# Performance work log

Measured on AMD Instinct MI355X. Metric: run time of the kernel, lower is better.

## Reference

```python
import jax, jax.numpy as jnp
import numpy as np

NUM_HEADS = 4
TEMPERATURE = 1.0
EDGE_WEIGHT = 0.5


def setup_inputs() -> dict:
    key = jax.random.key(0)
    k1, k2, k3 = jax.random.split(key, 3)
    x = jax.random.normal(k1, (4, 2048, 512), dtype=jnp.float32)
    gate_w = jax.random.normal(k2, (1, 1), dtype=jnp.float32)
    gate_b = jax.random.normal(k3, (1,), dtype=jnp.float32)
    return {"x": x, "gate_w": gate_w, "gate_b": gate_b}


def _forward(x, gate_w, gate_b):
    B, N, C = x.shape
    H = NUM_HEADS
    hd = C // H
    # F.normalize(x, dim=-1) with eps=1e-12
    norm = jnp.linalg.norm(x, axis=-1, keepdims=True)
    x_norm = x / jnp.maximum(norm, 1e-12)
    # multi-head cosine-sim attention
    xh = x_norm.reshape(B, N, H, hd).transpose(0, 2, 1, 3)  # (B,H,N,hd)
    sim = jnp.einsum("bhnd,bhmd->bhnm", xh, xh) / (hd ** 0.5 * TEMPERATURE)
    attn = jax.nn.softmax(sim, axis=-1)
    xv = x.reshape(B, N, H, hd).transpose(0, 2, 1, 3)  # (B,H,N,hd)
    x_refined = jnp.einsum("bhnm,bhmd->bhnd", attn, xv)
    x_refined = x_refined.transpose(0, 2, 1, 3).reshape(B, N, C)
    # edge-variance mask (no_grad in torch -> stop_gradient)
    diff = jnp.var(x, axis=-1, keepdims=True, ddof=1)  # (B,N,1), unbiased like torch
    edge_mask = jax.nn.sigmoid((diff - diff.mean()) / (jnp.std(diff, ddof=1) + 1e-6))
    edge_mask = jax.lax.stop_gradient(edge_mask)
    x_refined = (1.0 + EDGE_WEIGHT * edge_mask) * x_refined
    # scalar gate: Linear(1,1) + Sigmoid on global mean
    gate_input = x.mean(axis=1, keepdims=True).mean(axis=-1, keepdims=True)  # (B,1,1)
    gate = jax.nn.sigmoid(gate_input * gate_w[0, 0] + gate_b[0])
    x_refined = gate * x_refined
    return x + x_refined


def reference(x, gate_w, gate_b):
    return _forward(x, gate_w, gate_b)
```

## Files before the change

kernel.cpp:

```cpp
#include <hip/hip_runtime.h>
#include <stdint.h>

#define B_   4
#define N_   2048
#define C_   512
#define H_   4
#define HD_  128
#define BN_  (B_ * N_)
#define NIT_ 32
#define SCALE_LOG2E 0.1275129727595311f

typedef __attribute__((ext_vector_type(8))) short  short8;
typedef __attribute__((ext_vector_type(4))) unsigned short ushort4_t;
typedef __attribute__((ext_vector_type(4))) float  float4_t;
typedef __attribute__((ext_vector_type(8))) __bf16 bf16x8;

static __device__ __forceinline__ unsigned short f2bf(float f) {
  union { float f; uint32_t u; } v; v.f = f;
  uint32_t r = v.u + 0x7FFFu + ((v.u >> 16) & 1u);
  return (unsigned short)(r >> 16);
}

static __device__ __forceinline__ uint32_t cvtpk_bf16(float lo, float hi) {
  uint32_t r;
  asm("v_cvt_pk_bf16_f32 %0, %1, %2" : "=v"(r) : "v"(lo), "v"(hi));
  return r;
}

#if __has_builtin(__builtin_amdgcn_exp2f)
#define EXP2(x) __builtin_amdgcn_exp2f(x)
#else
#define EXP2(x) exp2f(x)
#endif

static __device__ __forceinline__ float4_t mfma16(short8 a, short8 b, float4_t c) {
  return __builtin_amdgcn_mfma_f32_16x16x32_bf16(
      __builtin_bit_cast(bf16x8, a), __builtin_bit_cast(bf16x8, b), c, 0, 0, 0);
}

#define GLOAD16(SRC, DST)                                               \
  __builtin_amdgcn_global_load_lds(                                     \
      (const __attribute__((address_space(1))) void*)(SRC),             \
      (__attribute__((address_space(3))) void*)(DST), 16, 0, 0)

__global__ __launch_bounds__(256) void k_stats(
    const float* __restrict__ x, unsigned short* __restrict__ xnq,
    float* __restrict__ diff, float* __restrict__ toksum) {
  int tok  = blockIdx.x * 4 + (threadIdx.x >> 6);
  int lane = threadIdx.x & 63;
  const float* xr = x + (size_t)tok * C_;
  float4_t a = *(const float4_t*)(xr + lane * 8);
  float4_t b = *(const float4_t*)(xr + lane * 8 + 4);
  float s = 0.f, ss = 0.f;
#pragma unroll
  for (int j = 0; j < 4; ++j) {
    s  += a[j] + b[j];
    ss += a[j] * a[j] + b[j] * b[j];
  }
#pragma unroll
  for (int o = 1; o < 64; o <<= 1) {
    s  += __shfl_xor(s, o);
    ss += __shfl_xor(ss, o);
  }
  float rn = 1.f / fmaxf(sqrtf(ss), 1e-12f);
  short8 o8;
#pragma unroll
  for (int j = 0; j < 4; ++j) {
    o8[j]     = (short)f2bf(a[j] * rn);
    o8[j + 4] = (short)f2bf(b[j] * rn);
  }
  *(short8*)(xnq + (size_t)tok * C_ + lane * 8) = o8;
  if (lane == 0) {
    diff[tok]   = (ss - s * s * (1.f / C_)) * (1.f / (C_ - 1));
    toksum[tok] = s;
  }
}

__global__ __launch_bounds__(256) void k_transpose(
    const float* __restrict__ x, unsigned short* __restrict__ xvT) {
  __shared__ float tr[HD_][65];
  int bh = blockIdx.x & 15, nt = blockIdx.x >> 4;
  int b = bh >> 2, h = bh & 3;
  int n0 = nt * 64, c0 = h * HD_;
  int t = threadIdx.x;
  int dm = (t & 31) * 4;
  int nr = t >> 5;
#pragma unroll
  for (int p = 0; p < 8; ++p) {
    int n = p * 8 + nr;
    float4_t v = *(const float4_t*)(x + ((size_t)(b * N_ + n0 + n)) * C_ + c0 + dm);
#pragma unroll
    for (int k = 0; k < 4; ++k) tr[dm + k][n] = v[k];
  }
  __syncthreads();
#pragma unroll
  for (int p = 0; p < 4; ++p) {
    int c = p * 256 + t;
    int d = c >> 3, nc = (c & 7) * 8;
    int P = ((d & 7) << 1) | ((d >> 3) & 1);
    int q0h = nc >> 2;
    ushort4_t h0, h1;
#pragma unroll
    for (int e = 0; e < 4; ++e) {
      h0[e] = f2bf(tr[d][nc + e]);
      h1[e] = f2bf(tr[d][nc + 4 + e]);
    }
    unsigned short* base = xvT + ((size_t)bh * HD_ + d) * N_ + n0;
    *(ushort4_t*)(base + (((q0h    ) ^ P) << 2)) = h0;
    *(ushort4_t*)(base + (((q0h + 1) ^ P) << 2)) = h1;
  }
}

__global__ __launch_bounds__(256) void k_finalize(
    const float* __restrict__ diff, const float* __restrict__ toksum,
    const float* __restrict__ gw, const float* __restrict__ gb,
    float* __restrict__ stats) {
  __shared__ float sh[4][8];
  int t = threadIdx.x, l = t & 63, w = t >> 6;
  float s1 = 0.f, s2 = 0.f;
  for (int i = t; i < BN_; i += 256) { float d = diff[i]; s1 += d; s2 += d * d; }
  float bs0 = 0.f, bs1 = 0.f, bs2 = 0.f, bs3 = 0.f;
  for (int i = t; i < N_; i += 256) {
    bs0 += toksum[i];          bs1 += toksum[N_ + i];
    bs2 += toksum[2 * N_ + i]; bs3 += toksum[3 * N_ + i];
  }
#pragma unroll
  for (int o = 1; o < 64; o <<= 1) {
    s1 += __shfl_xor(s1, o);  s2 += __shfl_xor(s2, o);
    bs0 += __shfl_xor(bs0, o); bs1 += __shfl_xor(bs1, o);
    bs2 += __shfl_xor(bs2, o); bs3 += __shfl_xor(bs3, o);
  }
  if (l == 0) {
    sh[w][0] = s1; sh[w][1] = s2;
    sh[w][2] = bs0; sh[w][3] = bs1; sh[w][4] = bs2; sh[w][5] = bs3;
  }
  __syncthreads();
  if (t == 0) {
    float S1 = sh[0][0] + sh[1][0] + sh[2][0] + sh[3][0];
    float S2 = sh[0][1] + sh[1][1] + sh[2][1] + sh[3][1];
    float mean = S1 / (float)BN_;
    float var  = (S2 - S1 * S1 / (float)BN_) / (float)(BN_ - 1);
    float rstd = 1.f / (sqrtf(var) + 1e-6f);
    stats[0] = mean; stats[1] = rstd;
    float w00 = gw[0], bb = gb[0];
#pragma unroll
    for (int q = 0; q < 4; ++q) {
      float bsum = sh[0][2 + q] + sh[1][2 + q] + sh[2][2 + q] + sh[3][2 + q];
      float gi = bsum / (float)(N_ * C_);
      stats[2 + q] = 1.f / (1.f + __expf(-(gi * w00 + bb)));
    }
  }
}

__global__ __launch_bounds__(256) void k_attn(
    const float* __restrict__ x, const unsigned short* __restrict__ xnq,
    const unsigned short* __restrict__ xvT, const float* __restrict__ diff,
    const float* __restrict__ stats, float* __restrict__ out) {
  __shared__ unsigned short sm[32768];
  int i  = blockIdx.x;
  int bh = ((i & 7) << 1) | ((i >> 3) & 1);
  int qt = i >> 4;
  int b = bh >> 2, h = bh & 3, c0 = h * HD_;
  int tid = threadIdx.x, w = tid >> 6, l = tid & 63;
  int g = l >> 4, r = l & 15;
  int r3 = (r >> 3) & 1;
  int q0 = qt * 64 + w * 16;

  short8 qf[4];
  const unsigned short* qbase = xnq + ((size_t)(b * N_ + q0)) * C_ + c0;
#pragma unroll
  for (int cs = 0; cs < 4; ++cs)
    qf[cs] = *(const short8*)(qbase + (size_t)r * C_ + g * 8 + cs * 32);

  float4_t acc[8];
  float ls = 0.f;
#pragma unroll
  for (int dt = 0; dt < 8; ++dt) acc[dt] = (float4_t){0.f, 0.f, 0.f, 0.f};

  auto stage = [&](int it, int cb) {
    const unsigned short* ks = xnq + ((size_t)(b * N_ + it * 64)) * C_ + c0;
    unsigned short* kd = &sm[cb * 8192];
#pragma unroll
    for (int jj = 0; jj < 4; ++jj) {
      int j = w * 4 + jj;
      int row = 4 * j + g;
      int ssl = r ^ (row & 15);
      GLOAD16(ks + (size_t)row * C_ + ssl * 8, kd + j * 512);
    }
    const unsigned short* vs = xvT + ((size_t)bh * HD_) * N_ + it * 64;
    unsigned short* vd = &sm[16384 + cb * 8192];
#pragma unroll
    for (int jj = 0; jj < 4; ++jj) {
      int j = w * 4 + jj;
      int d = 8 * j + (l >> 3);
      GLOAD16(vs + (size_t)d * N_ + (l & 7) * 8, vd + j * 512);
    }
  };

  stage(0, 0);
  __syncthreads();

  for (int it = 0; it < NIT_; ++it) {
    int cb = it & 1;
    if (it + 1 < NIT_) stage(it + 1, cb ^ 1);
    const unsigned short* K = &sm[cb * 8192];
    const unsigned short* V = &sm[16384 + cb * 8192];

    float4_t p[4];
#pragma unroll
    for (int t4 = 0; t4 < 4; ++t4) p[t4] = (float4_t){0.f, 0.f, 0.f, 0.f};

    __builtin_amdgcn_s_setprio(1);
#pragma unroll
    for (int t4 = 0; t4 < 4; ++t4) {
#pragma unroll
      for (int cs = 0; cs < 4; ++cs) {
        short8 kf = *(const short8*)(K + (size_t)(t4 * 16 + r) * 128 +
                                     ((g * 8 + cs * 32) ^ (r * 8)));
        p[t4] = mfma16(kf, qf[cs], p[t4]);
      }
    }
    __builtin_amdgcn_s_setprio(0);

    union { short8 s8; uint32_t u[4]; } pf[2];
#pragma unroll
    for (int t4 = 0; t4 < 4; ++t4) {
      float e0 = EXP2(p[t4][0] * SCALE_LOG2E);
      float e1 = EXP2(p[t4][1] * SCALE_LOG2E);
      float e2 = EXP2(p[t4][2] * SCALE_LOG2E);
      float e3 = EXP2(p[t4][3] * SCALE_LOG2E);
      ls += (e0 + e1) + (e2 + e3);
      pf[t4 >> 1].u[(t4 & 1) * 2 + 0] = cvtpk_bf16(e0, e1);
      pf[t4 >> 1].u[(t4 & 1) * 2 + 1] = cvtpk_bf16(e2, e3);
    }

    int X = ((r & 7) << 3) | (r3 << 2);
    __builtin_amdgcn_s_setprio(1);
#pragma unroll
    for (int dt = 0; dt < 8; ++dt) {
      const unsigned short* vrow = V + (size_t)(dt * 16 + r) * 64;
      union { short8 s8; ushort4_t h[2]; } vf0, vf1;
      vf0.h[0] = *(const ushort4_t*)(vrow + ((g * 4)      ^ X));
      vf0.h[1] = *(const ushort4_t*)(vrow + ((g * 4 + 16) ^ X));
      vf1.h[0] = *(const ushort4_t*)(vrow + ((g * 4 + 32) ^ X));
      vf1.h[1] = *(const ushort4_t*)(vrow + ((g * 4 + 48) ^ X));
      acc[dt] = mfma16(vf0.s8, pf[0].s8, acc[dt]);
      acc[dt] = mfma16(vf1.s8, pf[1].s8, acc[dt]);
    }
    __builtin_amdgcn_s_setprio(0);
    __syncthreads();
  }

  ls += __shfl_xor(ls, 16);
  ls += __shfl_xor(ls, 32);
  float mean = stats[0], rstd = stats[1], gate = stats[2 + b];
  int q = q0 + r;
  float dv = diff[b * N_ + q];
  float em = 1.f / (1.f + __expf(-(dv - mean) * rstd));
  float f  = gate * (1.f + 0.5f * em) / ls;
  const float* xr = x + ((size_t)(b * N_ + q)) * C_;
  float* orow = out + ((size_t)(b * N_ + q)) * C_;
#pragma unroll
  for (int dt = 0; dt < 8; ++dt) {
    int dcol = c0 + dt * 16 + g * 4;
    float4_t xin = *(const float4_t*)(xr + dcol);
    float4_t o;
#pragma unroll
    for (int j = 0; j < 4; ++j) o[j] = xin[j] + f * acc[dt][j];
    *(float4_t*)(orow + dcol) = o;
  }
}

extern "C" void kernel_launch(void* const* d_in, const int* in_sizes, int n_in,
                              void* d_out, int out_size, void* d_ws, size_t ws_size,
                              hipStream_t stream) {
  (void)in_sizes; (void)n_in; (void)out_size; (void)ws_size;
  const float* x  = (const float*)d_in[0];
  const float* gw = (const float*)d_in[1];
  const float* gb = (const float*)d_in[2];
  float* out = (float*)d_out;
  unsigned short* xnq = (unsigned short*)d_ws;
  unsigned short* xvT = xnq + (size_t)BN_ * C_;
  float* diff   = (float*)(xvT + (size_t)BN_ * C_);
  float* toksum = diff + BN_;
  float* stats  = toksum + BN_;
  hipLaunchKernelGGL(k_stats, dim3(BN_ / 4), dim3(256), 0, stream, x, xnq, diff, toksum);
  hipLaunchKernelGGL(k_transpose, dim3(512), dim3(256), 0, stream, x, xvT);
  hipLaunchKernelGGL(k_finalize, dim3(1), dim3(256), 0, stream, diff, toksum, gw, gb, stats);
  hipLaunchKernelGGL(k_attn, dim3(512), dim3(256), 0, stream, x, xnq, xvT, diff, stats, out);
}
```

Before: 77.43 us.

## Restructure attention to two waves with register-resident K and key-split reduction

The attention kernel now uses 128 threads per block. Each wave owns all 64 queries of the tile and handles a 32-key half, loading K fragments straight from global memory into registers rather than staging them through LDS. Only V is double-buffered in LDS, with a new swizzle that allows single 16-byte reads, and the transpose kernel writes V in that matching layout. The two waves' partial accumulators and row sums are combined through LDS at the end. The aim is more MFMA work per fragment load and less LDS traffic, at the cost of much higher register pressure, lower occupancy from launch_bounds(128,1), and an extra reduction step.

```diff
diff --git a/kernel.cpp b/kernel.cpp
--- a/kernel.cpp
+++ b/kernel.cpp
@@ -94,20 +94,16 @@
   }
   __syncthreads();
 #pragma unroll
-  for (int p = 0; p < 4; ++p) {
-    int c = p * 256 + t;
-    int d = c >> 3, nc = (c & 7) * 8;
-    int P = ((d & 7) << 1) | ((d >> 3) & 1);
-    int q0h = nc >> 2;
-    ushort4_t h0, h1;
-#pragma unroll
-    for (int e = 0; e < 4; ++e) {
-      h0[e] = f2bf(tr[d][nc + e]);
-      h1[e] = f2bf(tr[d][nc + 4 + e]);
-    }
-    unsigned short* base = xvT + ((size_t)bh * HD_ + d) * N_ + n0;
-    *(ushort4_t*)(base + (((q0h    ) ^ P) << 2)) = h0;
-    *(ushort4_t*)(base + (((q0h + 1) ^ P) << 2)) = h1;
+  for (int p4 = 0; p4 < 4; ++p4) {
+    int c = p4 * 256 + t;
+    int d = c >> 3, pb = c & 7;
+    int lg = pb ^ (d & 7);
+    int kbase = 32 * (lg >> 2) + 4 * (lg & 3);
+    short8 o8;
+#pragma unroll
+    for (int e = 0; e < 8; ++e)
+      o8[e] = (short)f2bf(tr[d][kbase + 16 * (e >> 2) + (e & 3)]);
+    *(short8*)(xvT + ((size_t)(bh * HD_ + d)) * N_ + n0 + pb * 8) = o8;
   }
 }
 
@@ -152,122 +148,193 @@
   }
 }
 
-__global__ __launch_bounds__(256) void k_attn(
+__global__ __launch_bounds__(128, 1) void k_attn(
     const float* __restrict__ x, const unsigned short* __restrict__ xnq,
     const unsigned short* __restrict__ xvT, const float* __restrict__ diff,
     const float* __restrict__ stats, float* __restrict__ out) {
-  __shared__ unsigned short sm[32768];
+  __shared__ unsigned short sm[16384];
   int i  = blockIdx.x;
   int bh = ((i & 7) << 1) | ((i >> 3) & 1);
   int qt = i >> 4;
   int b = bh >> 2, h = bh & 3, c0 = h * HD_;
   int tid = threadIdx.x, w = tid >> 6, l = tid & 63;
   int g = l >> 4, r = l & 15;
-  int r3 = (r >> 3) & 1;
-  int q0 = qt * 64 + w * 16;
-
-  short8 qf[4];
+  int q0 = qt * 64;
+
+  short8 qf[4][4];
   const unsigned short* qbase = xnq + ((size_t)(b * N_ + q0)) * C_ + c0;
 #pragma unroll
-  for (int cs = 0; cs < 4; ++cs)
-    qf[cs] = *(const short8*)(qbase + (size_t)r * C_ + g * 8 + cs * 32);
-
-  float4_t acc[8];
-  float ls = 0.f;
-#pragma unroll
-  for (int dt = 0; dt < 8; ++dt) acc[dt] = (float4_t){0.f, 0.f, 0.f, 0.f};
-
-  auto stage = [&](int it, int cb) {
-    const unsigned short* ks = xnq + ((size_t)(b * N_ + it * 64)) * C_ + c0;
-    unsigned short* kd = &sm[cb * 8192];
-#pragma unroll
-    for (int jj = 0; jj < 4; ++jj) {
-      int j = w * 4 + jj;
-      int row = 4 * j + g;
-      int ssl = r ^ (row & 15);
-      GLOAD16(ks + (size_t)row * C_ + ssl * 8, kd + j * 512);
-    }
-    const unsigned short* vs = xvT + ((size_t)bh * HD_) * N_ + it * 64;
-    unsigned short* vd = &sm[16384 + cb * 8192];
-#pragma unroll
-    for (int jj = 0; jj < 4; ++jj) {
-      int j = w * 4 + jj;
-      int d = 8 * j + (l >> 3);
-      GLOAD16(vs + (size_t)d * N_ + (l & 7) * 8, vd + j * 512);
-    }
+  for (int qs = 0; qs < 4; ++qs)
+#pragma unroll
+    for (int cs = 0; cs < 4; ++cs)
+      qf[qs][cs] = *(const short8*)(qbase + (size_t)(qs * 16 + r) * C_ + g * 8 + cs * 32);
+
+  short8 kf[2][4];
+  auto loadK = [&](int it) {
+    const unsigned short* kb =
+        xnq + ((size_t)(b * N_ + it * 64 + w * 32 + r)) * C_ + c0 + g * 8;
+#pragma unroll
+    for (int ks = 0; ks < 2; ++ks)
+#pragma unroll
+      for (int cs = 0; cs < 4; ++cs)
+        kf[ks][cs] = *(const short8*)(kb + ks * 16 * C_ + cs * 32);
   };
 
-  stage(0, 0);
-  __syncthreads();
-
+  auto stageV = [&](int it, int cb) {
+    const unsigned short* vsrc =
+        xvT + ((size_t)(bh * HD_ + w * 64 + (l >> 3))) * N_ + it * 64 + (l & 7) * 8;
+    unsigned short* vdst = &sm[cb * 8192 + w * 4096];
+#pragma unroll
+    for (int j = 0; j < 8; ++j)
+      GLOAD16(vsrc + (size_t)j * 8 * N_, vdst + j * 512);
+  };
+
+  float4_t acc[8][4];
+  float ls[4] = {0.f, 0.f, 0.f, 0.f};
+#pragma unroll
+  for (int dt = 0; dt < 8; ++dt)
+#pragma unroll
+    for (int qs = 0; qs < 4; ++qs) acc[dt][qs] = (float4_t){0.f, 0.f, 0.f, 0.f};
+
+  int vre = r * 64 + (((w * 4 + g) ^ (r & 7)) * 8);
+
+  loadK(0);
+  stageV(0, 0);
+  __syncthreads();
+
+#pragma unroll 2
   for (int it = 0; it < NIT_; ++it) {
     int cb = it & 1;
-    if (it + 1 < NIT_) stage(it + 1, cb ^ 1);
-    const unsigned short* K = &sm[cb * 8192];
-    const unsigned short* V = &sm[16384 + cb * 8192];
-
-    float4_t p[4];
-#pragma unroll
-    for (int t4 = 0; t4 < 4; ++t4) p[t4] = (float4_t){0.f, 0.f, 0.f, 0.f};
+    if (it + 1 < NIT_) stageV(it + 1, cb ^ 1);
+
+    float4_t p[2][4];
+#pragma unroll
+    for (int ks = 0; ks < 2; ++ks)
+#pragma unroll
+      for (int qs = 0; qs < 4; ++qs) p[ks][qs] = (float4_t){0.f, 0.f, 0.f, 0.f};
 
     __builtin_amdgcn_s_setprio(1);
 #pragma unroll
-    for (int t4 = 0; t4 < 4; ++t4) {
+    for (int ks = 0; ks < 2; ++ks)
 #pragma unroll
       for (int cs = 0; cs < 4; ++cs) {
-        short8 kf = *(const short8*)(K + (size_t)(t4 * 16 + r) * 128 +
-                                     ((g * 8 + cs * 32) ^ (r * 8)));
-        p[t4] = mfma16(kf, qf[cs], p[t4]);
-      }
-    }
+        short8 kfr = kf[ks][cs];
+#pragma unroll
+        for (int qs = 0; qs < 4; ++qs)
+          p[ks][qs] = mfma16(kfr, qf[qs][cs], p[ks][qs]);
+      }
     __builtin_amdgcn_s_setprio(0);
 
-    union { short8 s8; uint32_t u[4]; } pf[2];
-#pragma unroll
-    for (int t4 = 0; t4 < 4; ++t4) {
-      float e0 = EXP2(p[t4][0] * SCALE_LOG2E);
-      float e1 = EXP2(p[t4][1] * SCALE_LOG2E);
-      float e2 = EXP2(p[t4][2] * SCALE_LOG2E);
-      float e3 = EXP2(p[t4][3] * SCALE_LOG2E);
-      ls += (e0 + e1) + (e2 + e3);
-      pf[t4 >> 1].u[(t4 & 1) * 2 + 0] = cvtpk_bf16(e0, e1);
-      pf[t4 >> 1].u[(t4 & 1) * 2 + 1] = cvtpk_bf16(e2, e3);
-    }
-
-    int X = ((r & 7) << 3) | (r3 << 2);
+    if (it + 1 < NIT_) loadK(it + 1);
+
+    union { short8 s8; uint32_t u[4]; } pfq[4];
+#pragma unroll
+    for (int ks = 0; ks < 2; ++ks)
+#pragma unroll
+      for (int qs = 0; qs < 4; ++qs) {
+        float e0 = EXP2(p[ks][qs][0] * SCALE_LOG2E);
+        float e1 = EXP2(p[ks][qs][1] * SCALE_LOG2E);
+        float e2 = EXP2(p[ks][qs][2] * SCALE_LOG2E);
+        float e3 = EXP2(p[ks][qs][3] * SCALE_LOG2E);
+        ls[qs] += (e0 + e1) + (e2 + e3);
+        pfq[qs].u[ks * 2 + 0] = cvtpk_bf16(e0, e1);
+        pfq[qs].u[ks * 2 + 1] = cvtpk_bf16(e2, e3);
+      }
+
     __builtin_amdgcn_s_setprio(1);
 #pragma unroll
     for (int dt = 0; dt < 8; ++dt) {
-      const unsigned short* vrow = V + (size_t)(dt * 16 + r) * 64;
-      union { short8 s8; ushort4_t h[2]; } vf0, vf1;
-      vf0.h[0] = *(const ushort4_t*)(vrow + ((g * 4)      ^ X));
-      vf0.h[1] = *(const ushort4_t*)(vrow + ((g * 4 + 16) ^ X));
-      vf1.h[0] = *(const ushort4_t*)(vrow + ((g * 4 + 32) ^ X));
-      vf1.h[1] = *(const ushort4_t*)(vrow + ((g * 4 + 48) ^ X));
-      acc[dt] = mfma16(vf0.s8, pf[0].s8, acc[dt]);
-      acc[dt] = mfma16(vf1.s8, pf[1].s8, acc[dt]);
+      short8 vf = *(const short8*)(&sm[cb * 8192 + dt * 1024 + vre]);
+#pragma unroll
+      for (int qs = 0; qs < 4; ++qs)
+        acc[dt][qs] = mfma16(vf, pfq[qs].s8, acc[dt][qs]);
     }
     __builtin_amdgcn_s_setprio(0);
     __syncthreads();
   }
 
-  ls += __shfl_xor(ls, 16);
-  ls += __shfl_xor(ls, 32);
+#pragma unroll
+  for (int qs = 0; qs < 4; ++qs) {
+    ls[qs] += __shfl_xor(ls[qs], 16);
+    ls[qs] += __shfl_xor(ls[qs], 32);
+  }
+  float* smf = (float*)sm;
+  if (g == 0) {
+#pragma unroll
+    for (int qs = 0; qs < 4; ++qs) smf[w * 64 + qs * 16 + r] = ls[qs];
+  }
+  __syncthreads();
+  float lst[4];
+#pragma unroll
+  for (int qs = 0; qs < 4; ++qs)
+    lst[qs] = smf[qs * 16 + r] + smf[64 + qs * 16 + r];
+  __syncthreads();
+
+  float4_t* ex = (float4_t*)sm;
+  if (w == 0) {
+#pragma unroll
+    for (int k = 0; k < 4; ++k)
+#pragma unroll
+      for (int qs = 0; qs < 4; ++qs)
+        ex[l * 16 + ((k * 4 + qs) ^ (l & 15))] = acc[4 + k][qs];
+  } else {
+#pragma unroll
+    for (int k = 0; k < 4; ++k)
+#pragma unroll
+      for (int qs = 0; qs < 4; ++qs)
+        ex[1024 + l * 16 + ((k * 4 + qs) ^ (l & 15))] = acc[k][qs];
+  }
+  __syncthreads();
+  if (w == 0) {
+#pragma unroll
+    for (int k = 0; k < 4; ++k)
+#pragma unroll
+      for (int qs = 0; qs < 4; ++qs) {
+        float4_t o = ex[1024 + l * 16 + ((k * 4 + qs) ^ (l & 15))];
+#pragma unroll
+        for (int j = 0; j < 4; ++j) acc[k][qs][j] += o[j];
+      }
+  } else {
+#pragma unroll
+    for (int k = 0; k < 4; ++k)
+#pragma unroll
+      for (int qs = 0; qs < 4; ++qs) {
+        float4_t o = ex[l * 16 + ((k * 4 + qs) ^ (l & 15))];
+#pragma unroll
+        for (int j = 0; j < 4; ++j) acc[4 + k][qs][j] += o[j];
+      }
+  }
+
   float mean = stats[0], rstd = stats[1], gate = stats[2 + b];
-  int q = q0 + r;
-  float dv = diff[b * N_ + q];
-  float em = 1.f / (1.f + __expf(-(dv - mean) * rstd));
-  float f  = gate * (1.f + 0.5f * em) / ls;
-  const float* xr = x + ((size_t)(b * N_ + q)) * C_;
-  float* orow = out + ((size_t)(b * N_ + q)) * C_;
-#pragma unroll
-  for (int dt = 0; dt < 8; ++dt) {
-    int dcol = c0 + dt * 16 + g * 4;
-    float4_t xin = *(const float4_t*)(xr + dcol);
-    float4_t o;
-#pragma unroll
-    for (int j = 0; j < 4; ++j) o[j] = xin[j] + f * acc[dt][j];
-    *(float4_t*)(orow + dcol) = o;
+#pragma unroll
+  for (int qs = 0; qs < 4; ++qs) {
+    int q = q0 + qs * 16 + r;
+    float dv = diff[b * N_ + q];
+    float em = 1.f / (1.f + __expf(-(dv - mean) * rstd));
+    float f  = gate * (1.f + 0.5f * em) / lst[qs];
+    const float* xr = x + ((size_t)(b * N_ + q)) * C_;
+    float* orow = out + ((size_t)(b * N_ + q)) * C_;
+    if (w == 0) {
+#pragma unroll
+      for (int k = 0; k < 4; ++k) {
+        int dcol = c0 + k * 16 + g * 4;
+        float4_t xin = *(const float4_t*)(xr + dcol);
+        float4_t o;
+#pragma unroll
+        for (int j = 0; j < 4; ++j) o[j] = xin[j] + f * acc[k][qs][j];
+        *(float4_t*)(orow + dcol) = o;
+      }
+    } else {
+#pragma unroll
+      for (int k = 0; k < 4; ++k) {
+        int dcol = c0 + (4 + k) * 16 + g * 4;
+        float4_t xin = *(const float4_t*)(xr + dcol);
+        float4_t o;
+#pragma unroll
+        for (int j = 0; j < 4; ++j) o[j] = xin[j] + f * acc[4 + k][qs][j];
+        *(float4_t*)(orow + dcol) = o;
+      }
+    }
   }
 }
 
@@ -287,5 +354,5 @@
   hipLaunchKernelGGL(k_stats, dim3(BN_ / 4), dim3(256), 0, stream, x, xnq, diff, toksum);
   hipLaunchKernelGGL(k_transpose, dim3(512), dim3(256), 0, stream, x, xvT);
   hipLaunchKernelGGL(k_finalize, dim3(1), dim3(256), 0, stream, diff, toksum, gw, gb, stats);
-  hipLaunchKernelGGL(k_attn, dim3(512), dim3(256), 0, stream, x, xnq, xvT, diff, stats, out);
-}
+  hipLaunchKernelGGL(k_attn, dim3(512), dim3(128), 0, stream, x, xnq, xvT, diff, stats, out);
+}
```

After: 77.19 us. Within noise of the previous version (-0.3%).
